# Kernel tuning notes

Hardware: AMD Instinct MI355X
Metric: run time of the kernel (lower is better)

## Reference

```python
import jax, jax.numpy as jnp
import numpy as np

N_NODES = 50000
N_EDGES = 800000


def setup_inputs() -> dict:
    key = jax.random.key(0)
    ks = jax.random.split(key, 12)
    x = jax.random.normal(ks[0], (N_NODES, 500), dtype=jnp.float32)
    edge_src = jax.random.randint(ks[1], (N_EDGES,), 0, N_NODES, dtype=jnp.int32)
    edge_dst = jax.random.randint(ks[2], (N_EDGES,), 0, N_NODES, dtype=jnp.int32)
    edge_vals = jax.random.uniform(ks[3], (N_EDGES,), dtype=jnp.float32) * 0.1
    def w(k, fan_in, fan_out):
        s = 1.0 / np.sqrt(fan_in)
        return jax.random.uniform(k, (fan_in, fan_out), dtype=jnp.float32, minval=-s, maxval=s)
    W1 = w(ks[4], 500, 128)
    b1 = jnp.zeros((128,), jnp.float32)
    W2 = w(ks[5], 128, 64)
    b2 = jnp.zeros((64,), jnp.float32)
    W3 = w(ks[6], 64, 16)
    b3 = jnp.zeros((16,), jnp.float32)
    We = w(ks[7], 64, 64)
    be = jnp.zeros((64,), jnp.float32)
    return {"x": x, "edge_vals": edge_vals, "W1": W1, "b1": b1, "W2": W2,
            "b2": b2, "W3": W3, "b3": b3, "We": We, "be": be,
            "edge_src": edge_src, "edge_dst": edge_dst}


def reference(x, edge_vals, W1, b1, W2, b2, W3, b3, We, be, edge_src, edge_dst):
    n = x.shape[0]

    def gcn_layer(h, W, b):
        # GraphConvolution: support = h @ W ; out = spmm(adj, support) + b
        support = h @ W                                   # [N, d_out]
        msg = support[edge_dst] * edge_vals[:, None]      # [E, d_out]
        agg = jax.ops.segment_sum(msg, edge_src, num_segments=n)
        return agg + b

    h = jax.nn.relu(gcn_layer(x, W1, b1))
    # dropout omitted (eval mode, training=False)
    h = jax.nn.relu(gcn_layer(h, W2, b2))
    out1 = jax.nn.log_softmax(gcn_layer(h, W3, b3), axis=1)
    out2 = h @ We + be
    return (out1, out2)
```

## Files before the change

kernel.cpp:

```cpp
#include <hip/hip_runtime.h>
#include <hip/hip_bf16.h>
#include <math.h>

#define N_NODES 50000
#define N_EDGES 800000

typedef __attribute__((ext_vector_type(8))) short bf16x8;
typedef __attribute__((ext_vector_type(4))) float f32x4;

__device__ inline unsigned short f2bf(float f) {
    unsigned u = __float_as_uint(f);
    unsigned r = (u + 0x7fffu + ((u >> 16) & 1u)) >> 16;
    return (unsigned short)r;
}

__device__ inline bf16x8 pack8(float4 a0, float4 a1) {
    union { __hip_bfloat162 h2[4]; bf16x8 v; } u;
    u.h2[0] = __float22bfloat162_rn(make_float2(a0.x, a0.y));
    u.h2[1] = __float22bfloat162_rn(make_float2(a0.z, a0.w));
    u.h2[2] = __float22bfloat162_rn(make_float2(a1.x, a1.y));
    u.h2[3] = __float22bfloat162_rn(make_float2(a1.z, a1.w));
    return u.v;
}

__global__ __launch_bounds__(256) void convert_hist_kernel(
    const float* __restrict__ W1, const float* __restrict__ W2,
    const float* __restrict__ We, const float* __restrict__ W3,
    unsigned short* __restrict__ W1frag, unsigned short* __restrict__ W2frag,
    unsigned short* __restrict__ Wcfrag,
    const int* __restrict__ src, int* __restrict__ counts)
{
    if (blockIdx.x < 308) {
        int t = blockIdx.x * 256 + threadIdx.x;
        if (t < 65536) {
            int h = t >> 15;
            int r1 = t & 32767;
            int j = r1 >> 13;
            int r2 = r1 & 8191;
            int s = r2 >> 9;
            int r3 = r2 & 511;
            int lane = r3 >> 3, jj = r3 & 7;
            int k = s * 32 + (lane >> 4) * 8 + jj;
            int n = h * 64 + j * 16 + (lane & 15);
            float v = (k < 500) ? W1[k * 128 + n] : 0.0f;
            W1frag[t] = f2bf(v);
        } else if (t < 73728) {
            int t2 = t - 65536;
            int j = t2 >> 11;
            int s = (t2 >> 9) & 3;
            int lane = (t2 >> 3) & 63, jj = t2 & 7;
            int k = s * 32 + (lane >> 4) * 8 + jj;
            int n = j * 16 + (lane & 15);
            W2frag[t2] = f2bf(W2[k * 64 + n]);
        } else {
            int t3 = t - 73728;
            int j = t3 >> 10;
            int s = (t3 >> 9) & 1;
            int lane = (t3 >> 3) & 63, jj = t3 & 7;
            int k = s * 32 + (lane >> 4) * 8 + jj;
            int n = j * 16 + (lane & 15);
            float v = (n < 64) ? We[k * 64 + n] : W3[k * 16 + (n - 64)];
            Wcfrag[t3] = f2bf(v);
        }
    } else {
        int e = (blockIdx.x - 308) * 256 + threadIdx.x;
        if (e < N_EDGES) atomicAdd(&counts[src[e]], 1);
    }
}

__global__ __launch_bounds__(1024) void scan_kernel(
    const int* __restrict__ counts, int* __restrict__ row_ptr,
    int* __restrict__ cursor)
{
    constexpr int Q = N_NODES / 4;
    const int t = threadIdx.x;
    const int lane = t & 63, wave = t >> 6;
    __shared__ int wsum[16];
    __shared__ int carry_s;
    int carry = 0;
    const int4* c4 = reinterpret_cast<const int4*>(counts);
    int4* rp4 = reinterpret_cast<int4*>(row_ptr);
    int4* cu4 = reinterpret_cast<int4*>(cursor);

    for (int base = 0; base < Q; base += 4096) {
        int4 v[4];
        int ls[5];
        ls[0] = 0;
#pragma unroll
        for (int k = 0; k < 4; ++k) {
            const int g = base + t * 4 + k;
            if (g < Q) v[k] = c4[g];
            else       v[k] = make_int4(0, 0, 0, 0);
            ls[k + 1] = ls[k] + v[k].x + v[k].y + v[k].z + v[k].w;
        }
        const int s = ls[4];

        int incl = s;
#pragma unroll
        for (int off = 1; off < 64; off <<= 1) {
            int n = __shfl_up(incl, off, 64);
            if (lane >= off) incl += n;
        }
        if (lane == 63) wsum[wave] = incl;
        __syncthreads();
        if (t < 16) {
            int w = wsum[t];
            int inc = w;
#pragma unroll
            for (int off = 1; off < 16; off <<= 1) {
                int n = __shfl_up(inc, off, 64);
                if (t >= off) inc += n;
            }
            wsum[t] = inc - w;
            if (t == 15) carry_s = inc;
        }
        __syncthreads();
        const int e0 = carry + wsum[wave] + (incl - s);
#pragma unroll
        for (int k = 0; k < 4; ++k) {
            const int g = base + t * 4 + k;
            if (g < Q) {
                const int b0 = e0 + ls[k];
                int4 r;
                r.x = b0;
                r.y = r.x + v[k].x;
                r.z = r.y + v[k].y;
                r.w = r.z + v[k].z;
                rp4[g] = r;
                cu4[g] = r;
            }
        }
        carry += carry_s;
        __syncthreads();
    }
    if (t == 0) row_ptr[N_NODES] = carry;
}

__global__ __launch_bounds__(256) void fill_kernel(
    const int* __restrict__ src, const int* __restrict__ dst,
    const float* __restrict__ vals, int* __restrict__ cursor,
    int2* __restrict__ pairs)
{
    int e = blockIdx.x * 256 + threadIdx.x;
    if (e >= N_EDGES) return;
    int pos = atomicAdd(&cursor[src[e]], 1);
    pairs[pos] = make_int2(dst[e], __float_as_int(vals[e]));
}

__global__ __launch_bounds__(256, 2) void gemm1_mfma_kernel(
    const float* __restrict__ A,
    const unsigned short* __restrict__ W1frag,
    unsigned short* __restrict__ C)
{
    __shared__ __align__(16) unsigned short Bs[32768];

    const int t = threadIdx.x;
    const int h  = blockIdx.x & 1;
    const int br = blockIdx.x >> 1;
    const int lane = t & 63;
    const int wave = t >> 6;
    const int r = lane & 15, q = lane >> 4;

    {
        const uint4* src = reinterpret_cast<const uint4*>(W1frag + h * 32768);
        uint4* dst = reinterpret_cast<uint4*>(Bs);
#pragma unroll
        for (int i = 0; i < 16; ++i)
            dst[t + i * 256] = src[t + i * 256];
    }
    __syncthreads();

    const int col0 = h * 64;

    for (int c = br * 4 + wave; c < 3125; c += 1024) {
        const float* ap = A + (size_t)(c * 16 + r) * 500;

        f32x4 acc[4];
#pragma unroll
        for (int j = 0; j < 4; ++j) acc[j] = {0.f, 0.f, 0.f, 0.f};

#pragma unroll 4
        for (int s = 0; s < 16; ++s) {
            const int kb = s * 32 + q * 8;
            const int k0 = kb < 496 ? kb : 496;
            const int k1 = (kb + 4) < 496 ? (kb + 4) : 496;
            float4 a0 = *reinterpret_cast<const float4*>(ap + k0);
            float4 a1 = *reinterpret_cast<const float4*>(ap + k1);
            bf16x8 af = pack8(a0, a1);
#pragma unroll
            for (int j = 0; j < 4; ++j) {
                bf16x8 b = *reinterpret_cast<const bf16x8*>(
                    &Bs[(size_t)((j * 16 + s) * 64 + lane) * 8]);
                acc[j] = __builtin_amdgcn_mfma_f32_16x16x32_bf16(af, b, acc[j], 0, 0, 0);
            }
        }

#pragma unroll
        for (int reg = 0; reg < 4; ++reg) {
            const int grow = c * 16 + q * 4 + reg;
#pragma unroll
            for (int j = 0; j < 4; ++j)
                C[(size_t)grow * 128 + col0 + j * 16 + r] = f2bf(acc[j][reg]);
        }
    }
}

__global__ __launch_bounds__(256) void gather128_gemm2_kernel(
    const unsigned short* __restrict__ support, const int2* __restrict__ pairs,
    const int* __restrict__ row_ptr, const float* __restrict__ b1,
    const unsigned short* __restrict__ W2frag,
    unsigned short* __restrict__ sup2)
{
    __shared__ __align__(16) unsigned short Bs[8192];
    __shared__ __align__(16) unsigned short h1s[16 * 136];

    const int t = threadIdx.x;
    const int lane = t & 63, wave = t >> 6;
    const int f = lane & 15, e = lane >> 4;

    {
        const uint4* src = reinterpret_cast<const uint4*>(W2frag);
        uint4* dst = reinterpret_cast<uint4*>(Bs);
#pragma unroll
        for (int i = 0; i < 4; ++i)
            dst[t + i * 256] = src[t + i * 256];
    }

    const float4 ba = *reinterpret_cast<const float4*>(b1 + f * 8);
    const float4 bb = *reinterpret_cast<const float4*>(b1 + f * 8 + 4);
    const float bias[8] = {ba.x, ba.y, ba.z, ba.w, bb.x, bb.y, bb.z, bb.w};

    const int node0 = blockIdx.x * 16 + wave * 4;

    for (int nn = 0; nn < 4; ++nn) {
        const int node = node0 + nn;
        int i = row_ptr[node] + e;
        const int end = row_ptr[node + 1];

        float acc[8] = {};
        for (; i + 4 < end; i += 8) {
            int2 p0 = pairs[i], p1 = pairs[i + 4];
            float v0 = __int_as_float(p0.y), v1 = __int_as_float(p1.y);
            uint4 r0 = *reinterpret_cast<const uint4*>(support + (size_t)p0.x * 128 + f * 8);
            uint4 r1 = *reinterpret_cast<const uint4*>(support + (size_t)p1.x * 128 + f * 8);
            unsigned w0[4] = {r0.x, r0.y, r0.z, r0.w};
            unsigned w1[4] = {r1.x, r1.y, r1.z, r1.w};
#pragma unroll
            for (int j = 0; j < 4; ++j) {
                acc[2 * j]     += __uint_as_float(w0[j] << 16) * v0;
                acc[2 * j + 1] += __uint_as_float(w0[j] & 0xffff0000u) * v0;
                acc[2 * j]     += __uint_as_float(w1[j] << 16) * v1;
                acc[2 * j + 1] += __uint_as_float(w1[j] & 0xffff0000u) * v1;
            }
        }
        if (i < end) {
            int2 p = pairs[i];
            float v = __int_as_float(p.y);
            uint4 r = *reinterpret_cast<const uint4*>(support + (size_t)p.x * 128 + f * 8);
            unsigned w[4] = {r.x, r.y, r.z, r.w};
#pragma unroll
            for (int j = 0; j < 4; ++j) {
                acc[2 * j]     += __uint_as_float(w[j] << 16) * v;
                acc[2 * j + 1] += __uint_as_float(w[j] & 0xffff0000u) * v;
            }
        }
#pragma unroll
        for (int j = 0; j < 8; ++j) {
            acc[j] += __shfl_xor(acc[j], 16, 64);
            acc[j] += __shfl_xor(acc[j], 32, 64);
        }
        if (e == 0) {
            unsigned short hv[8];
#pragma unroll
            for (int j = 0; j < 8; ++j) {
                float v = acc[j] + bias[j];
                hv[j] = f2bf(v > 0.0f ? v : 0.0f);
            }
            *reinterpret_cast<uint4*>(&h1s[(wave * 4 + nn) * 136 + f * 8]) =
                *reinterpret_cast<uint4*>(hv);
        }
    }
    __syncthreads();

    f32x4 acc2 = {0.f, 0.f, 0.f, 0.f};
#pragma unroll
    for (int s = 0; s < 4; ++s) {
        bf16x8 af = *reinterpret_cast<const bf16x8*>(&h1s[f * 136 + (s * 4 + e) * 8]);
        bf16x8 b = *reinterpret_cast<const bf16x8*>(
            &Bs[(size_t)((wave * 4 + s) * 64 + lane) * 8]);
        acc2 = __builtin_amdgcn_mfma_f32_16x16x32_bf16(af, b, acc2, 0, 0, 0);
    }
#pragma unroll
    for (int reg = 0; reg < 4; ++reg) {
        const int grow = blockIdx.x * 16 + e * 4 + reg;
        sup2[(size_t)grow * 64 + wave * 16 + f] = f2bf(acc2[reg]);
    }
}

__global__ __launch_bounds__(256) void gather64_gemm3_kernel(
    const unsigned short* __restrict__ support, const int2* __restrict__ pairs,
    const int* __restrict__ row_ptr, const float* __restrict__ b2,
    const unsigned short* __restrict__ Wcfrag, const float* __restrict__ be,
    float* __restrict__ out2, float* __restrict__ sup3)
{
    __shared__ __align__(16) unsigned short Bs[5120];
    __shared__ __align__(16) unsigned short h2s[16 * 68];

    const int t = threadIdx.x;
    const int lane = t & 63, wave = t >> 6;
    const int f = lane & 7, e = lane >> 3;

    {
        const uint4* src = reinterpret_cast<const uint4*>(Wcfrag);
        uint4* dst = reinterpret_cast<uint4*>(Bs);
#pragma unroll
        for (int i = 0; i < 2; ++i)
            dst[t + i * 256] = src[t + i * 256];
        if (t < 128) dst[512 + t] = src[512 + t];
    }

    const float4 ba = *reinterpret_cast<const float4*>(b2 + f * 8);
    const float4 bb = *reinterpret_cast<const float4*>(b2 + f * 8 + 4);
    const float bias[8] = {ba.x, ba.y, ba.z, ba.w, bb.x, bb.y, bb.z, bb.w};

    const int node0 = blockIdx.x * 16 + wave * 4;

    for (int nn = 0; nn < 4; ++nn) {
        const int node = node0 + nn;
        int i = row_ptr[node] + e;
        const int end = row_ptr[node + 1];

        float acc[8] = {};
        for (; i + 8 < end; i += 16) {
            int2 p0 = pairs[i], p1 = pairs[i + 8];
            float v0 = __int_as_float(p0.y), v1 = __int_as_float(p1.y);
            uint4 r0 = *reinterpret_cast<const uint4*>(support + (size_t)p0.x * 64 + f * 8);
            uint4 r1 = *reinterpret_cast<const uint4*>(support + (size_t)p1.x * 64 + f * 8);
            unsigned w0[4] = {r0.x, r0.y, r0.z, r0.w};
            unsigned w1[4] = {r1.x, r1.y, r1.z, r1.w};
#pragma unroll
            for (int j = 0; j < 4; ++j) {
                acc[2 * j]     += __uint_as_float(w0[j] << 16) * v0;
                acc[2 * j + 1] += __uint_as_float(w0[j] & 0xffff0000u) * v0;
                acc[2 * j]     += __uint_as_float(w1[j] << 16) * v1;
                acc[2 * j + 1] += __uint_as_float(w1[j] & 0xffff0000u) * v1;
            }
        }
        if (i < end) {
            int2 p = pairs[i];
            float v = __int_as_float(p.y);
            uint4 r = *reinterpret_cast<const uint4*>(support + (size_t)p.x * 64 + f * 8);
            unsigned w[4] = {r.x, r.y, r.z, r.w};
#pragma unroll
            for (int j = 0; j < 4; ++j) {
                acc[2 * j]     += __uint_as_float(w[j] << 16) * v;
                acc[2 * j + 1] += __uint_as_float(w[j] & 0xffff0000u) * v;
            }
        }
#pragma unroll
        for (int j = 0; j < 8; ++j) {
            acc[j] += __shfl_xor(acc[j], 8, 64);
            acc[j] += __shfl_xor(acc[j], 16, 64);
            acc[j] += __shfl_xor(acc[j], 32, 64);
        }
        if (e == 0) {
            unsigned short hv[8];
#pragma unroll
            for (int j = 0; j < 8; ++j) {
                float v = acc[j] + bias[j];
                hv[j] = f2bf(v > 0.0f ? v : 0.0f);
            }
            *reinterpret_cast<uint4*>(&h2s[(wave * 4 + nn) * 68 + f * 8]) =
                *reinterpret_cast<uint4*>(hv);
        }
    }
    __syncthreads();

    const int r = lane & 15, q = lane >> 4;
    const bf16x8 af0 = *reinterpret_cast<const bf16x8*>(&h2s[r * 68 + q * 8]);
    const bf16x8 af1 = *reinterpret_cast<const bf16x8*>(&h2s[r * 68 + (4 + q) * 8]);

    f32x4 accA = {0.f, 0.f, 0.f, 0.f};
    accA = __builtin_amdgcn_mfma_f32_16x16x32_bf16(
        af0, *reinterpret_cast<const bf16x8*>(&Bs[(size_t)((wave * 2 + 0) * 64 + lane) * 8]),
        accA, 0, 0, 0);
    accA = __builtin_amdgcn_mfma_f32_16x16x32_bf16(
        af1, *reinterpret_cast<const bf16x8*>(&Bs[(size_t)((wave * 2 + 1) * 64 + lane) * 8]),
        accA, 0, 0, 0);
    const float bev = be[wave * 16 + r];
#pragma unroll
    for (int reg = 0; reg < 4; ++reg) {
        const int grow = blockIdx.x * 16 + q * 4 + reg;
        out2[(size_t)grow * 64 + wave * 16 + r] = accA[reg] + bev;
    }

    if (wave == 0) {
        f32x4 accB = {0.f, 0.f, 0.f, 0.f};
        accB = __builtin_amdgcn_mfma_f32_16x16x32_bf16(
            af0, *reinterpret_cast<const bf16x8*>(&Bs[(size_t)((4 * 2 + 0) * 64 + lane) * 8]),
            accB, 0, 0, 0);
        accB = __builtin_amdgcn_mfma_f32_16x16x32_bf16(
            af1, *reinterpret_cast<const bf16x8*>(&Bs[(size_t)((4 * 2 + 1) * 64 + lane) * 8]),
            accB, 0, 0, 0);
#pragma unroll
        for (int reg = 0; reg < 4; ++reg) {
            const int grow = blockIdx.x * 16 + q * 4 + reg;
            sup3[(size_t)grow * 16 + r] = accB[reg];
        }
    }
}

__global__ __launch_bounds__(256) void gather16_lsm_kernel(
    const float* __restrict__ sup3, const int2* __restrict__ pairs,
    const int* __restrict__ row_ptr, const float* __restrict__ b3,
    float* __restrict__ out1)
{
    const int node = blockIdx.x * 4 + (threadIdx.x >> 6);
    const int lane = threadIdx.x & 63;
    const int f = lane & 3, e = lane >> 2;
    int i = row_ptr[node] + e;
    const int end = row_ptr[node + 1];

    float4 acc = {0, 0, 0, 0};
    for (; i + 16 < end; i += 32) {
        int2 p0 = pairs[i], p1 = pairs[i + 16];
        float v0 = __int_as_float(p0.y), v1 = __int_as_float(p1.y);
        float4 m0 = *reinterpret_cast<const float4*>(sup3 + (size_t)p0.x * 16 + f * 4);
        float4 m1 = *reinterpret_cast<const float4*>(sup3 + (size_t)p1.x * 16 + f * 4);
        acc.x += m0.x * v0 + m1.x * v1;
        acc.y += m0.y * v0 + m1.y * v1;
        acc.z += m0.z * v0 + m1.z * v1;
        acc.w += m0.w * v0 + m1.w * v1;
    }
    if (i < end) {
        int2 p = pairs[i];
        float v = __int_as_float(p.y);
        float4 m = *reinterpret_cast<const float4*>(sup3 + (size_t)p.x * 16 + f * 4);
        acc.x += m.x * v; acc.y += m.y * v; acc.z += m.z * v; acc.w += m.w * v;
    }
#pragma unroll
    for (int off = 4; off < 64; off <<= 1) {
        acc.x += __shfl_xor(acc.x, off, 64);
        acc.y += __shfl_xor(acc.y, off, 64);
        acc.z += __shfl_xor(acc.z, off, 64);
        acc.w += __shfl_xor(acc.w, off, 64);
    }
    const float4 b = *reinterpret_cast<const float4*>(b3 + f * 4);
    float a0 = acc.x + b.x, a1 = acc.y + b.y, a2 = acc.z + b.z, a3 = acc.w + b.w;
    float mx = fmaxf(fmaxf(a0, a1), fmaxf(a2, a3));
    mx = fmaxf(mx, __shfl_xor(mx, 1, 64));
    mx = fmaxf(mx, __shfl_xor(mx, 2, 64));
    float s = expf(a0 - mx) + expf(a1 - mx) + expf(a2 - mx) + expf(a3 - mx);
    s += __shfl_xor(s, 1, 64);
    s += __shfl_xor(s, 2, 64);
    const float lse = mx + logf(s);
    if (e == 0) {
        float4 o = {a0 - lse, a1 - lse, a2 - lse, a3 - lse};
        *reinterpret_cast<float4*>(out1 + (size_t)node * 16 + f * 4) = o;
    }
}

extern "C" void kernel_launch(void* const* d_in, const int* in_sizes, int n_in,
                              void* d_out, int out_size, void* d_ws, size_t ws_size,
                              hipStream_t stream)
{
    const float* x         = (const float*)d_in[0];
    const float* edge_vals = (const float*)d_in[1];
    const float* W1 = (const float*)d_in[2];
    const float* b1 = (const float*)d_in[3];
    const float* W2 = (const float*)d_in[4];
    const float* b2 = (const float*)d_in[5];
    const float* W3 = (const float*)d_in[6];
    const float* b3 = (const float*)d_in[7];
    const float* We = (const float*)d_in[8];
    const float* be = (const float*)d_in[9];
    const int* esrc = (const int*)d_in[10];
    const int* edst = (const int*)d_in[11];

    float* out1 = (float*)d_out;
    float* out2 = (float*)d_out + (size_t)N_NODES * 16;

    char* ws = (char*)d_ws;
    float* bufA    = (float*)(ws);
    float* bufB    = (float*)(ws + 25600000);
    float* bufC    = (float*)(ws + 51200000);
    int*   counts  = (int*)  (ws + 54400000);
    int*   row_ptr = (int*)  (ws + 54600064);
    int*   cursor  = (int*)  (ws + 54800128);
    int2*  pairs   = (int2*) (ws + 55000192);

    unsigned short* W1frag = (unsigned short*)bufC;
    unsigned short* W2frag = (unsigned short*)((char*)bufC + 131072);
    unsigned short* Wcfrag = (unsigned short*)((char*)bufC + 147456);

    unsigned short* sup1bf = (unsigned short*)bufA;
    unsigned short* sup2bf = (unsigned short*)bufB;
    float*          sup3   = bufA;

    const int EB  = (N_EDGES + 255) / 256;
    const int GN  = N_NODES / 4;
    const int GB  = N_NODES / 16;

    hipMemsetAsync(counts, 0, (size_t)N_NODES * 4, stream);
    convert_hist_kernel<<<308 + EB, 256, 0, stream>>>(
        W1, W2, We, W3, W1frag, W2frag, Wcfrag, esrc, counts);
    scan_kernel<<<1, 1024, 0, stream>>>(counts, row_ptr, cursor);
    fill_kernel<<<EB, 256, 0, stream>>>(esrc, edst, edge_vals, cursor, pairs);

    gemm1_mfma_kernel<<<512, 256, 0, stream>>>(x, W1frag, sup1bf);

    gather128_gemm2_kernel<<<GB, 256, 0, stream>>>(
        sup1bf, pairs, row_ptr, b1, W2frag, sup2bf);

    gather64_gemm3_kernel<<<GB, 256, 0, stream>>>(
        sup2bf, pairs, row_ptr, b2, Wcfrag, be, out2, sup3);

    gather16_lsm_kernel<<<GN, 256, 0, stream>>>(sup3, pairs, row_ptr, b3, out1);
}
```

Baseline: 358.9 us.

## Fuse CSR build prep into one cooperative kernel with grid syncs

Replaces the memset, weight-convert/histogram, single-block scan and fill launches with one cooperative kernel of 1024 blocks that uses grid.sync between phases. It targets launch overhead and the inter-kernel gaps of four small launches. The trade-off is that the scan now runs on one 256-thread block while every other block waits at a grid barrier, and it adds three grid-wide syncs. The old multi-launch path is kept as a fallback if the cooperative launch fails.

```diff
diff --git a/kernel.cpp b/kernel.cpp
--- a/kernel.cpp
+++ b/kernel.cpp
@@ -1,6 +1,9 @@
 #include <hip/hip_runtime.h>
 #include <hip/hip_bf16.h>
+#include <hip/hip_cooperative_groups.h>
 #include <math.h>
+
+namespace cg = cooperative_groups;
 
 #define N_NODES 50000
 #define N_EDGES 800000
@@ -23,6 +26,140 @@
     return u.v;
 }
 
+__device__ inline void convert_weights_at(
+    int t,
+    const float* __restrict__ W1, const float* __restrict__ W2,
+    const float* __restrict__ We, const float* __restrict__ W3,
+    unsigned short* __restrict__ W1frag, unsigned short* __restrict__ W2frag,
+    unsigned short* __restrict__ Wcfrag)
+{
+    if (t < 65536) {
+        int h = t >> 15;
+        int r1 = t & 32767;
+        int j = r1 >> 13;
+        int r2 = r1 & 8191;
+        int s = r2 >> 9;
+        int r3 = r2 & 511;
+        int lane = r3 >> 3, jj = r3 & 7;
+        int k = s * 32 + (lane >> 4) * 8 + jj;
+        int n = h * 64 + j * 16 + (lane & 15);
+        float v = (k < 500) ? W1[k * 128 + n] : 0.0f;
+        W1frag[t] = f2bf(v);
+    } else if (t < 73728) {
+        int t2 = t - 65536;
+        int j = t2 >> 11;
+        int s = (t2 >> 9) & 3;
+        int lane = (t2 >> 3) & 63, jj = t2 & 7;
+        int k = s * 32 + (lane >> 4) * 8 + jj;
+        int n = j * 16 + (lane & 15);
+        W2frag[t2] = f2bf(W2[k * 64 + n]);
+    } else if (t < 78848) {
+        int t3 = t - 73728;
+        int j = t3 >> 10;
+        int s = (t3 >> 9) & 1;
+        int lane = (t3 >> 3) & 63, jj = t3 & 7;
+        int k = s * 32 + (lane >> 4) * 8 + jj;
+        int n = j * 16 + (lane & 15);
+        float v = (n < 64) ? We[k * 64 + n] : W3[k * 16 + (n - 64)];
+        Wcfrag[t3] = f2bf(v);
+    }
+}
+
+__global__ __launch_bounds__(256, 4) void prep_coop_kernel(
+    const float* __restrict__ W1, const float* __restrict__ W2,
+    const float* __restrict__ We, const float* __restrict__ W3,
+    unsigned short* __restrict__ W1frag, unsigned short* __restrict__ W2frag,
+    unsigned short* __restrict__ Wcfrag,
+    const int* __restrict__ esrc, const int* __restrict__ edst,
+    const float* __restrict__ evals,
+    int* __restrict__ counts, int* __restrict__ row_ptr,
+    int* __restrict__ cursor, int2* __restrict__ pairs)
+{
+    cg::grid_group grid = cg::this_grid();
+    const int NT = gridDim.x * 256;
+    const int gtid = blockIdx.x * 256 + threadIdx.x;
+
+    __shared__ int wsum[4];
+    __shared__ int carry_s;
+
+    for (int i = gtid; i < N_NODES; i += NT) counts[i] = 0;
+    grid.sync();
+
+    convert_weights_at(gtid, W1, W2, We, W3, W1frag, W2frag, Wcfrag);
+    for (int e = gtid; e < N_EDGES; e += NT)
+        atomicAdd(&counts[esrc[e]], 1);
+    grid.sync();
+
+    if (blockIdx.x == 0) {
+        constexpr int Q = N_NODES / 4;
+        const int t = threadIdx.x;
+        const int lane = t & 63, wave = t >> 6;
+        int carry = 0;
+        const int4* c4 = reinterpret_cast<const int4*>(counts);
+        int4* rp4 = reinterpret_cast<int4*>(row_ptr);
+        int4* cu4 = reinterpret_cast<int4*>(cursor);
+
+        for (int base = 0; base < Q; base += 1024) {
+            int4 v[4];
+            int ls[5];
+            ls[0] = 0;
+#pragma unroll
+            for (int k = 0; k < 4; ++k) {
+                const int g = base + t * 4 + k;
+                if (g < Q) v[k] = c4[g];
+                else       v[k] = make_int4(0, 0, 0, 0);
+                ls[k + 1] = ls[k] + v[k].x + v[k].y + v[k].z + v[k].w;
+            }
+            const int s = ls[4];
+
+            int incl = s;
+#pragma unroll
+            for (int off = 1; off < 64; off <<= 1) {
+                int n = __shfl_up(incl, off, 64);
+                if (lane >= off) incl += n;
+            }
+            if (lane == 63) wsum[wave] = incl;
+            __syncthreads();
+            if (t < 4) {
+                int w = wsum[t];
+                int inc = w;
+#pragma unroll
+                for (int off = 1; off < 4; off <<= 1) {
+                    int n = __shfl_up(inc, off, 64);
+                    if (t >= off) inc += n;
+                }
+                wsum[t] = inc - w;
+                if (t == 3) carry_s = inc;
+            }
+            __syncthreads();
+            const int e0 = carry + wsum[wave] + (incl - s);
+#pragma unroll
+            for (int k = 0; k < 4; ++k) {
+                const int g = base + t * 4 + k;
+                if (g < Q) {
+                    const int b0 = e0 + ls[k];
+                    int4 r;
+                    r.x = b0;
+                    r.y = r.x + v[k].x;
+                    r.z = r.y + v[k].y;
+                    r.w = r.z + v[k].z;
+                    rp4[g] = r;
+                    cu4[g] = r;
+                }
+            }
+            carry += carry_s;
+            __syncthreads();
+        }
+        if (t == 0) row_ptr[N_NODES] = carry;
+    }
+    grid.sync();
+
+    for (int e = gtid; e < N_EDGES; e += NT) {
+        int pos = atomicAdd(&cursor[esrc[e]], 1);
+        pairs[pos] = make_int2(edst[e], __float_as_int(evals[e]));
+    }
+}
+
 __global__ __launch_bounds__(256) void convert_hist_kernel(
     const float* __restrict__ W1, const float* __restrict__ W2,
     const float* __restrict__ We, const float* __restrict__ W3,
@@ -32,36 +169,7 @@
 {
     if (blockIdx.x < 308) {
         int t = blockIdx.x * 256 + threadIdx.x;
-        if (t < 65536) {
-            int h = t >> 15;
-            int r1 = t & 32767;
-            int j = r1 >> 13;
-            int r2 = r1 & 8191;
-            int s = r2 >> 9;
-            int r3 = r2 & 511;
-            int lane = r3 >> 3, jj = r3 & 7;
-            int k = s * 32 + (lane >> 4) * 8 + jj;
-            int n = h * 64 + j * 16 + (lane & 15);
-            float v = (k < 500) ? W1[k * 128 + n] : 0.0f;
-            W1frag[t] = f2bf(v);
-        } else if (t < 73728) {
-            int t2 = t - 65536;
-            int j = t2 >> 11;
-            int s = (t2 >> 9) & 3;
-            int lane = (t2 >> 3) & 63, jj = t2 & 7;
-            int k = s * 32 + (lane >> 4) * 8 + jj;
-            int n = j * 16 + (lane & 15);
-            W2frag[t2] = f2bf(W2[k * 64 + n]);
-        } else {
-            int t3 = t - 73728;
-            int j = t3 >> 10;
-            int s = (t3 >> 9) & 1;
-            int lane = (t3 >> 3) & 63, jj = t3 & 7;
-            int k = s * 32 + (lane >> 4) * 8 + jj;
-            int n = j * 16 + (lane & 15);
-            float v = (n < 64) ? We[k * 64 + n] : W3[k * 16 + (n - 64)];
-            Wcfrag[t3] = f2bf(v);
-        }
+        convert_weights_at(t, W1, W2, We, W3, W1frag, W2frag, Wcfrag);
     } else {
         int e = (blockIdx.x - 308) * 256 + threadIdx.x;
         if (e < N_EDGES) atomicAdd(&counts[src[e]], 1);
@@ -501,11 +609,22 @@
     const int GN  = N_NODES / 4;
     const int GB  = N_NODES / 16;
 
-    hipMemsetAsync(counts, 0, (size_t)N_NODES * 4, stream);
-    convert_hist_kernel<<<308 + EB, 256, 0, stream>>>(
-        W1, W2, We, W3, W1frag, W2frag, Wcfrag, esrc, counts);
-    scan_kernel<<<1, 1024, 0, stream>>>(counts, row_ptr, cursor);
-    fill_kernel<<<EB, 256, 0, stream>>>(esrc, edst, edge_vals, cursor, pairs);
+    {
+        void* args[] = {
+            (void*)&W1, (void*)&W2, (void*)&We, (void*)&W3,
+            (void*)&W1frag, (void*)&W2frag, (void*)&Wcfrag,
+            (void*)&esrc, (void*)&edst, (void*)&edge_vals,
+            (void*)&counts, (void*)&row_ptr, (void*)&cursor, (void*)&pairs};
+        hipError_t cerr = hipLaunchCooperativeKernel(
+            (void*)prep_coop_kernel, dim3(1024), dim3(256), args, 0, stream);
+        if (cerr != hipSuccess) {
+            hipMemsetAsync(counts, 0, (size_t)N_NODES * 4, stream);
+            convert_hist_kernel<<<308 + EB, 256, 0, stream>>>(
+                W1, W2, We, W3, W1frag, W2frag, Wcfrag, esrc, counts);
+            scan_kernel<<<1, 1024, 0, stream>>>(counts, row_ptr, cursor);
+            fill_kernel<<<EB, 256, 0, stream>>>(esrc, edst, edge_vals, cursor, pairs);
+        }
+    }
 
     gemm1_mfma_kernel<<<512, 256, 0, stream>>>(x, W1frag, sup1bf);
 
```

After: 642.0 us. 78.9% more time.
